# Kernel optimization log

Measured on AMD Instinct MI355X. Metric: run time of the kernel, lower is better.

The kernel has to match this reference:

```python
import jax, jax.numpy as jnp
import numpy as np

N_QUBITS = 14
LAYERS = 2
BATCH = 64
N_PARAMS = 5 * N_QUBITS * LAYERS  # 140
TWO_PI = 2.0 * np.pi
C64 = jnp.complex64


def _rx(t):  # t: [B] -> [B,2,2]
    c = jnp.cos(t * 0.5).astype(C64)
    s = (-1j * jnp.sin(t * 0.5)).astype(C64)
    return jnp.stack([jnp.stack([c, s], -1), jnp.stack([s, c], -1)], -2)


def _ry(t):
    c = jnp.cos(t * 0.5).astype(C64)
    s = jnp.sin(t * 0.5).astype(C64)
    return jnp.stack([jnp.stack([c, -s], -1), jnp.stack([s, c], -1)], -2)


def _rz(t):
    e = jnp.exp(-0.5j * t.astype(C64))
    z = jnp.zeros_like(e)
    return jnp.stack([jnp.stack([e, z], -1), jnp.stack([z, jnp.conj(e)], -1)], -2)


def _apply_1q(psi, U, axis):
    # psi: [B, 2, 2, ...]; U: [B,2,2]; apply U on given tensor axis (>=1).
    psi = jnp.moveaxis(psi, axis, -1)
    psi = jnp.einsum('b...j,bij->b...i', psi, U)
    return jnp.moveaxis(psi, -1, axis)


def _apply_crx(psi, theta, ctrl, tgt):
    # controlled-RX: apply RX(theta) on target only in the control=1 subspace.
    U = _rx(theta)
    psi0 = jax.lax.index_in_dim(psi, 0, axis=ctrl + 1, keepdims=False)
    psi1 = jax.lax.index_in_dim(psi, 1, axis=ctrl + 1, keepdims=False)
    t2 = tgt if tgt < ctrl else tgt - 1  # target axis after removing ctrl axis
    psi1 = _apply_1q(psi1, U, t2 + 1)
    return jnp.stack([psi0, psi1], axis=ctrl + 1)


def _circuit(angles):
    # angles: [B, N_PARAMS] -> features [B, 3*N_QUBITS] (X, Y, Z expvals)
    B = angles.shape[0]
    n = N_QUBITS
    psi = jnp.zeros((B, 2 ** n), C64).at[:, 0].set(1.0)
    psi = psi.reshape((B,) + (2,) * n)
    idx = 0
    for _ in range(LAYERS):
        for i in range(n):
            psi = _apply_1q(psi, _rx(angles[:, idx]), i + 1)
            psi = _apply_1q(psi, _ry(angles[:, idx + 1]), i + 1)
            psi = _apply_1q(psi, _rz(angles[:, idx + 2]), i + 1)
            idx += 3
        for i in range(n):  # forward CRX ring
            psi = _apply_crx(psi, angles[:, idx], i, (i + 1) % n)
            idx += 1
        for i in range(n - 1, -1, -1):  # backward CRX ring
            psi = _apply_crx(psi, angles[:, idx], i, (i - 1) % n)
            idx += 1
    conj = jnp.conj(psi)
    probs = jnp.real(psi * conj)
    axes_all = tuple(range(1, n + 1))
    xs, ys, zs = [], [], []
    for w in range(n):
        flip = jnp.flip(psi, axis=w + 1)  # X action: swap |0>,|1> on wire w
        xs.append(jnp.real(jnp.sum(conj * flip, axis=axes_all)))
        fshape = [1] * (n + 1)
        fshape[w + 1] = 2
        f = jnp.array([-1j, 1j], C64).reshape(fshape)  # Y phases
        ys.append(jnp.real(jnp.sum(conj * f * flip, axis=axes_all)))
        p = probs.sum(axis=tuple(a for a in axes_all if a != w + 1))  # [B,2]
        zs.append(p[:, 0] - p[:, 1])
    return jnp.stack(xs + ys + zs, axis=1).astype(jnp.float32)


def setup_inputs() -> dict:
    key = jax.random.key(0)
    k1, k2 = jax.random.split(key)
    params = jax.random.normal(k1, (BATCH, N_PARAMS), dtype=jnp.float32)
    base_params = jax.random.uniform(k2, (N_PARAMS,), dtype=jnp.float32) * TWO_PI
    return {"params": params, "base_params": base_params}


def reference(params, base_params):
    angles = jax.nn.sigmoid(params + base_params[None, :]) * TWO_PI
    return _circuit(angles)
```

## Files before the change

### kernel.cpp

```cpp
#include <hip/hip_runtime.h>

#define NP 140
#define NT 1024

typedef float2 f2;

__device__ __forceinline__ float sigmoid2pi(float x) {
    return 6.28318530717958647692f / (1.0f + __expf(-x));
}
__device__ __forceinline__ f2 cmulf(f2 a, f2 b) {
    return make_float2(a.x * b.x - a.y * b.y, a.x * b.y + a.y * b.x);
}
__device__ __forceinline__ f2 comb(f2 ca, f2 m, f2 cb, f2 o) {
    return make_float2(ca.x * m.x - ca.y * m.y + cb.x * o.x - cb.y * o.y,
                       ca.x * m.y + ca.y * m.x + cb.x * o.y + cb.y * o.x);
}
__device__ __forceinline__ f2 rxmix(float ch, float sh, f2 m, f2 o) {
    return make_float2(ch * m.x + sh * o.y, ch * m.y - sh * o.x);
}
__device__ __forceinline__ float wsum(float v) {
    v += __shfl_down(v, 32); v += __shfl_down(v, 16); v += __shfl_down(v, 8);
    v += __shfl_down(v, 4);  v += __shfl_down(v, 2);  v += __shfl_down(v, 1);
    return v;
}

constexpr unsigned rot14c(unsigned x, int d) {
    return ((x << d) | (x >> (14 - d))) & 16383u;
}
constexpr unsigned koffc(unsigned i, int d) {
    unsigned c = rot14c(i, d);
    return (c + (c >> 4) + (c >> 8)) * 8u;
}

#define P_B0(OP) OP(0,1) OP(2,3) OP(4,5) OP(6,7) OP(8,9) OP(10,11) OP(12,13) OP(14,15)
#define P_B1(OP) OP(0,2) OP(1,3) OP(4,6) OP(5,7) OP(8,10) OP(9,11) OP(12,14) OP(13,15)
#define P_B2(OP) OP(0,4) OP(1,5) OP(2,6) OP(3,7) OP(8,12) OP(9,13) OP(10,14) OP(11,15)
#define P_B3(OP) OP(0,8) OP(1,9) OP(2,10) OP(3,11) OP(4,12) OP(5,13) OP(6,14) OP(7,15)
#define P_32(OP) OP(8,12) OP(9,13) OP(10,14) OP(11,15)
#define P_21(OP) OP(4,6) OP(5,7) OP(12,14) OP(13,15)
#define P_10(OP) OP(2,3) OP(6,7) OP(10,11) OP(14,15)
#define P_23(OP) OP(4,12) OP(5,13) OP(6,14) OP(7,15)
#define P_12(OP) OP(2,6) OP(3,7) OP(10,14) OP(11,15)
#define P_01(OP) OP(1,3) OP(5,7) OP(9,11) OP(13,15)

#define OP_RX(a_, b_) { f2 ta_ = st##a_; \
    st##a_ = rxmix(ch_, sh_, ta_, st##b_); st##b_ = rxmix(ch_, sh_, st##b_, ta_); }
#define OP_G1(a_, b_) { f2 ta_ = st##a_, tb_ = st##b_; \
    st##a_ = comb(u00_, ta_, u01_, tb_); st##b_ = comb(u10_, ta_, u11_, tb_); }
#define OP_MX(a_, b_) { \
    sx += st##a_.x * st##b_.x + st##a_.y * st##b_.y; \
    sy += st##a_.x * st##b_.y - st##a_.y * st##b_.x; \
    sz += st##a_.x * st##a_.x + st##a_.y * st##a_.y - st##b_.x * st##b_.x - st##b_.y * st##b_.y; }

#define CRX_CL(CI_, PL) { f2 cs_ = csh2[CI_]; float ch_ = cs_.x, sh_ = cs_.y; PL(OP_RX) }
#define CRX_SEL0(CI_) { f2 cs_ = csh2[CI_]; float ch_ = cs_.x, sh_ = cs_.y; \
    if (tid & 1) { P_B3(OP_RX) } }
#define CRX_W512(CI_) { f2 cs_ = csh2[CI_]; float ch_ = cs_.x, sh_ = cs_.y; \
    if (tid & 512) { P_B0(OP_RX) } }
#define G1Q(q_, PL) { float4 ga_ = g1v[q_][0], gb_ = g1v[q_][1]; \
    f2 u00_ = make_float2(ga_.x, ga_.y), u01_ = make_float2(ga_.z, ga_.w); \
    f2 u10_ = make_float2(gb_.x, gb_.y), u11_ = make_float2(gb_.z, gb_.w); PL(OP_G1) }
#define MEAS(w_, PL) { float sx = 0.f, sy = 0.f, sz = 0.f; PL(OP_MX) \
    sx = wsum(2.f * sx); sy = wsum(2.f * sy); sz = wsum(sz); \
    if ((tid & 63) == 0) { red[w_][tid >> 6][0] = sx; red[w_][tid >> 6][1] = sy; red[w_][tid >> 6][2] = sz; } }

#define XPOSE(D_) { \
    __syncthreads(); \
    { char* wb_ = (char*)exb + (unsigned)(tid * 17 + (tid >> 4)) * 8u; \
      *(f2*)(wb_ +   0) = st0;  *(f2*)(wb_ +   8) = st1;  *(f2*)(wb_ +  16) = st2;  *(f2*)(wb_ +  24) = st3; \
      *(f2*)(wb_ +  32) = st4;  *(f2*)(wb_ +  40) = st5;  *(f2*)(wb_ +  48) = st6;  *(f2*)(wb_ +  56) = st7; \
      *(f2*)(wb_ +  64) = st8;  *(f2*)(wb_ +  72) = st9;  *(f2*)(wb_ +  80) = st10; *(f2*)(wb_ +  88) = st11; \
      *(f2*)(wb_ +  96) = st12; *(f2*)(wb_ + 104) = st13; *(f2*)(wb_ + 112) = st14; *(f2*)(wb_ + 120) = st15; } \
    __syncthreads(); \
    { unsigned aw_ = (unsigned)tid << 4; \
      unsigned rt_ = ((aw_ << (D_)) | (aw_ >> (14 - (D_)))) & 16383u; \
      const char* rb_ = (const char*)exb + (rt_ + (rt_ >> 4) + (rt_ >> 8)) * 8u; \
      st0  = *(const f2*)(rb_ + koffc(0,  D_)); st1  = *(const f2*)(rb_ + koffc(1,  D_)); \
      st2  = *(const f2*)(rb_ + koffc(2,  D_)); st3  = *(const f2*)(rb_ + koffc(3,  D_)); \
      st4  = *(const f2*)(rb_ + koffc(4,  D_)); st5  = *(const f2*)(rb_ + koffc(5,  D_)); \
      st6  = *(const f2*)(rb_ + koffc(6,  D_)); st7  = *(const f2*)(rb_ + koffc(7,  D_)); \
      st8  = *(const f2*)(rb_ + koffc(8,  D_)); st9  = *(const f2*)(rb_ + koffc(9,  D_)); \
      st10 = *(const f2*)(rb_ + koffc(10, D_)); st11 = *(const f2*)(rb_ + koffc(11, D_)); \
      st12 = *(const f2*)(rb_ + koffc(12, D_)); st13 = *(const f2*)(rb_ + koffc(13, D_)); \
      st14 = *(const f2*)(rb_ + koffc(14, D_)); st15 = *(const f2*)(rb_ + koffc(15, D_)); } }

__global__
__attribute__((amdgpu_flat_work_group_size(1024, 1024), amdgpu_waves_per_eu(4, 4)))
void qfe_kernel(const float* __restrict__ params,
                const float* __restrict__ base,
                float* __restrict__ out)
{
    __shared__ f2 exb[17472];
    __shared__ f2 v1c[14][2];
    __shared__ float4 g1v[14][2];
    __shared__ f2 csh2[56];
    __shared__ float red[14][16][3];

    const int b = blockIdx.x;
    const int tid = threadIdx.x;

    if (tid < 14) {
        int q = tid, a = 3 * q;
        float t1 = sigmoid2pi(params[b * NP + a] + base[a]);
        float t2 = sigmoid2pi(params[b * NP + a + 1] + base[a + 1]);
        float t3 = sigmoid2pi(params[b * NP + a + 2] + base[a + 2]);
        float s1, c1, s2, c2, s3, c3;
        __sincosf(0.5f * t1, &s1, &c1);
        __sincosf(0.5f * t2, &s2, &c2);
        __sincosf(0.5f * t3, &s3, &c3);
        f2 m00 = make_float2(c2 * c1, s2 * s1);
        f2 m10 = make_float2(s2 * c1, -c2 * s1);
        f2 em = make_float2(c3, -s3), ep = make_float2(c3, s3);
        v1c[q][0] = cmulf(em, m00);
        v1c[q][1] = cmulf(ep, m10);
    } else if (tid >= 64 && tid < 78) {
        int q = tid - 64, a = 70 + 3 * q;
        float t1 = sigmoid2pi(params[b * NP + a] + base[a]);
        float t2 = sigmoid2pi(params[b * NP + a + 1] + base[a + 1]);
        float t3 = sigmoid2pi(params[b * NP + a + 2] + base[a + 2]);
        float s1, c1, s2, c2, s3, c3;
        __sincosf(0.5f * t1, &s1, &c1);
        __sincosf(0.5f * t2, &s2, &c2);
        __sincosf(0.5f * t3, &s3, &c3);
        f2 m00 = make_float2(c2 * c1, s2 * s1);
        f2 m01 = make_float2(-s2 * c1, -c2 * s1);
        f2 m10 = make_float2(s2 * c1, -c2 * s1);
        f2 m11 = make_float2(c2 * c1, -s2 * s1);
        f2 em = make_float2(c3, -s3), ep = make_float2(c3, s3);
        f2 u00 = cmulf(em, m00), u01 = cmulf(em, m01);
        f2 u10 = cmulf(ep, m10), u11 = cmulf(ep, m11);
        g1v[q][0] = make_float4(u00.x, u00.y, u01.x, u01.y);
        g1v[q][1] = make_float4(u10.x, u10.y, u11.x, u11.y);
    } else if (tid >= 128 && tid < 184) {
        int s = tid - 128;
        int layer = s / 28, k = s % 28;
        int aidx = layer * 70 + (k < 14 ? 42 + k : 56 + (k - 14));
        float th = sigmoid2pi(params[b * NP + aidx] + base[aidx]);
        float sh, ch;
        __sincosf(0.5f * th, &sh, &ch);
        csh2[s] = make_float2(ch, sh);
    }
    __syncthreads();

    f2 F = v1c[0][tid & 1];
    F = cmulf(F, v1c[13][(tid >> 1) & 1]);
    F = cmulf(F, v1c[12][(tid >> 2) & 1]);
    F = cmulf(F, v1c[11][(tid >> 3) & 1]);
    F = cmulf(F, v1c[10][(tid >> 4) & 1]);
    F = cmulf(F, v1c[9][(tid >> 5) & 1]);
    F = cmulf(F, v1c[8][(tid >> 6) & 1]);
    F = cmulf(F, v1c[7][(tid >> 7) & 1]);
    F = cmulf(F, v1c[6][(tid >> 8) & 1]);
    F = cmulf(F, v1c[5][(tid >> 9) & 1]);

    f2 st0, st1, st2, st3, st4, st5, st6, st7, st8, st9, st10, st11, st12, st13, st14, st15;
    st0 = cmulf(F, v1c[1][0]);  st8 = cmulf(F, v1c[1][1]);
    st4 = cmulf(st0, v1c[2][1]); st12 = cmulf(st8, v1c[2][1]);
    st0 = cmulf(st0, v1c[2][0]); st8  = cmulf(st8, v1c[2][0]);
    st2  = cmulf(st0, v1c[3][1]); st6  = cmulf(st4,  v1c[3][1]);
    st10 = cmulf(st8, v1c[3][1]); st14 = cmulf(st12, v1c[3][1]);
    st0  = cmulf(st0, v1c[3][0]); st4  = cmulf(st4,  v1c[3][0]);
    st8  = cmulf(st8, v1c[3][0]); st12 = cmulf(st12, v1c[3][0]);
    st1  = cmulf(st0,  v1c[4][1]); st3  = cmulf(st2,  v1c[4][1]);
    st5  = cmulf(st4,  v1c[4][1]); st7  = cmulf(st6,  v1c[4][1]);
    st9  = cmulf(st8,  v1c[4][1]); st11 = cmulf(st10, v1c[4][1]);
    st13 = cmulf(st12, v1c[4][1]); st15 = cmulf(st14, v1c[4][1]);
    st0  = cmulf(st0,  v1c[4][0]); st2  = cmulf(st2,  v1c[4][0]);
    st4  = cmulf(st4,  v1c[4][0]); st6  = cmulf(st6,  v1c[4][0]);
    st8  = cmulf(st8,  v1c[4][0]); st10 = cmulf(st10, v1c[4][0]);
    st12 = cmulf(st12, v1c[4][0]); st14 = cmulf(st14, v1c[4][0]);

    CRX_SEL0(0) CRX_CL(1, P_32) CRX_CL(2, P_21) CRX_CL(3, P_10)
    XPOSE(10)
    CRX_SEL0(4) CRX_CL(5, P_32) CRX_CL(6, P_21) CRX_CL(7, P_10)
    XPOSE(10)
    CRX_SEL0(8) CRX_CL(9, P_32) CRX_CL(10, P_21) CRX_CL(11, P_10)
    XPOSE(11)
    CRX_CL(12, P_32) CRX_CL(13, P_21) CRX_CL(14, P_23)
    XPOSE(3)
    CRX_CL(15, P_01) CRX_CL(16, P_12) CRX_CL(17, P_23)
    XPOSE(4)
    CRX_W512(18) CRX_CL(19, P_01) CRX_CL(20, P_12) CRX_CL(21, P_23)
    XPOSE(4)
    CRX_W512(22) CRX_CL(23, P_01) CRX_CL(24, P_12) CRX_CL(25, P_23)
    XPOSE(4)
    CRX_W512(26) CRX_CL(27, P_01)

    G1Q(0, P_B0) G1Q(13, P_B1) G1Q(12, P_B2) G1Q(11, P_B3)
    XPOSE(10)
    G1Q(1, P_B3) G1Q(2, P_B2) G1Q(3, P_B1) G1Q(4, P_B0)
    CRX_SEL0(28) CRX_CL(29, P_32) CRX_CL(30, P_21) CRX_CL(31, P_10)
    XPOSE(10)
    G1Q(5, P_B3) G1Q(6, P_B2) G1Q(7, P_B1) G1Q(8, P_B0)
    CRX_SEL0(32) CRX_CL(33, P_32) CRX_CL(34, P_21) CRX_CL(35, P_10)
    XPOSE(10)
    G1Q(9, P_B3) G1Q(10, P_B2)
    CRX_SEL0(36) CRX_CL(37, P_32) CRX_CL(38, P_21) CRX_CL(39, P_10)
    XPOSE(11)
    CRX_CL(40, P_32) CRX_CL(41, P_21) CRX_CL(42, P_23)
    XPOSE(3)
    CRX_CL(43, P_01) CRX_CL(44, P_12) CRX_CL(45, P_23)
    XPOSE(4)
    CRX_W512(46) CRX_CL(47, P_01) CRX_CL(48, P_12) CRX_CL(49, P_23)
    XPOSE(4)
    CRX_W512(50) CRX_CL(51, P_01) CRX_CL(52, P_12) CRX_CL(53, P_23)
    XPOSE(4)
    CRX_W512(54) CRX_CL(55, P_01)

    MEAS(0, P_B0) MEAS(13, P_B1) MEAS(12, P_B2) MEAS(11, P_B3)
    XPOSE(10)
    MEAS(1, P_B3) MEAS(2, P_B2) MEAS(3, P_B1) MEAS(4, P_B0)
    XPOSE(10)
    MEAS(5, P_B3) MEAS(6, P_B2) MEAS(7, P_B1) MEAS(8, P_B0)
    XPOSE(10)
    MEAS(9, P_B3) MEAS(10, P_B2)

    __syncthreads();
    if (tid < 42) {
        int comp = tid / 14, w = tid % 14;
        float s = 0.f;
        #pragma unroll
        for (int k = 0; k < 16; ++k) s += red[w][k][comp];
        out[b * 42 + comp * 14 + w] = s;
    }
}

extern "C" void kernel_launch(void* const* d_in, const int* in_sizes, int n_in,
                              void* d_out, int out_size, void* d_ws, size_t ws_size,
                              hipStream_t stream) {
    const float* params = (const float*)d_in[0];
    const float* base   = (const float*)d_in[1];
    float* out = (float*)d_out;
    const int B = in_sizes[0] / NP;
    qfe_kernel<<<B, NT, 0, stream>>>(params, base, out);
}
```

Baseline: 70.84 us.

## Use DPP lane exchanges for low-lane qubits to cut LDS transposes

```diff
diff --git a/kernel.cpp b/kernel.cpp
--- a/kernel.cpp
+++ b/kernel.cpp
@@ -18,9 +18,33 @@
 __device__ __forceinline__ f2 rxmix(float ch, float sh, f2 m, f2 o) {
     return make_float2(ch * m.x + sh * o.y, ch * m.y - sh * o.x);
 }
+__device__ __forceinline__ float rfl(float x) {
+    return __int_as_float(__builtin_amdgcn_readfirstlane(__float_as_int(x)));
+}
+
+#define XOR1 0xB1
+#define XOR2 0x4E
+#define XOR8 0x128
+template<int CTRL>
+__device__ __forceinline__ float xdpp(float v) {
+    return __int_as_float(__builtin_amdgcn_update_dpp(0, __float_as_int(v), CTRL, 0xF, 0xF, true));
+}
+template<int CTRL>
+__device__ __forceinline__ f2 xchg(f2 v) { return make_float2(xdpp<CTRL>(v.x), xdpp<CTRL>(v.y)); }
+__device__ __forceinline__ f2 xchg4(f2 v) {
+    return make_float2(
+        __int_as_float(__builtin_amdgcn_ds_swizzle(__float_as_int(v.x), 0x101F)),
+        __int_as_float(__builtin_amdgcn_ds_swizzle(__float_as_int(v.y), 0x101F)));
+}
+
+template<int CTRL>
+__device__ __forceinline__ float dppadd(float v) {
+    int t = __builtin_amdgcn_update_dpp(0, __float_as_int(v), CTRL, 0xF, 0xF, true);
+    return v + __int_as_float(t);
+}
 __device__ __forceinline__ float wsum(float v) {
-    v += __shfl_down(v, 32); v += __shfl_down(v, 16); v += __shfl_down(v, 8);
-    v += __shfl_down(v, 4);  v += __shfl_down(v, 2);  v += __shfl_down(v, 1);
+    v = dppadd<0x118>(v); v = dppadd<0x114>(v); v = dppadd<0x112>(v);
+    v = dppadd<0x111>(v); v = dppadd<0x142>(v); v = dppadd<0x143>(v);
     return v;
 }
 
@@ -42,27 +66,57 @@
 #define P_23(OP) OP(4,12) OP(5,13) OP(6,14) OP(7,15)
 #define P_12(OP) OP(2,6) OP(3,7) OP(10,14) OP(11,15)
 #define P_01(OP) OP(1,3) OP(5,7) OP(9,11) OP(13,15)
+#define ALL16(OP) OP(0) OP(1) OP(2) OP(3) OP(4) OP(5) OP(6) OP(7) OP(8) OP(9) OP(10) OP(11) OP(12) OP(13) OP(14) OP(15)
+#define HI8(OP)  OP(8) OP(9) OP(10) OP(11) OP(12) OP(13) OP(14) OP(15)
 
 #define OP_RX(a_, b_) { f2 ta_ = st##a_; \
     st##a_ = rxmix(ch_, sh_, ta_, st##b_); st##b_ = rxmix(ch_, sh_, st##b_, ta_); }
+#define OP_RXD(i_) { f2 o_ = xchg<CT_>(st##i_); st##i_ = rxmix(chx_, shx_, st##i_, o_); }
 #define OP_G1(a_, b_) { f2 ta_ = st##a_, tb_ = st##b_; \
     st##a_ = comb(u00_, ta_, u01_, tb_); st##b_ = comb(u10_, ta_, u11_, tb_); }
+#define OP_G1D(i_) { f2 o_ = xchg<CT_>(st##i_); st##i_ = comb(ca_, st##i_, cb_, o_); }
+
+#define CRX_LL(CI_, PL) { f2 cs_ = csh2[CI_]; float ch_ = rfl(cs_.x), sh_ = rfl(cs_.y); PL(OP_RX) }
+#define CRX_SELC(CI_, SELM_, PL) { f2 cs_ = csh2[CI_]; \
+    float ch_ = (tid & SELM_) ? cs_.x : 1.0f, sh_ = (tid & SELM_) ? cs_.y : 0.0f; PL(OP_RX) }
+#define CRX_SELW(CI_, PL) { f2 cs_ = csh2[CI_]; float ch_ = rfl(cs_.x), sh_ = rfl(cs_.y); \
+    if (tid & 512) { PL(OP_RX) } }
+#define CRX_DPPSEL(CI_, SELM_, CTV_) { f2 cs_ = csh2[CI_]; \
+    float chx_ = (tid & SELM_) ? cs_.x : 1.0f, shx_ = (tid & SELM_) ? cs_.y : 0.0f; \
+    constexpr int CT_ = CTV_; ALL16(OP_RXD) }
+#define CRX_DPPH8(CI_, CTV_) { f2 cs_ = csh2[CI_]; \
+    float chx_ = rfl(cs_.x), shx_ = rfl(cs_.y); \
+    constexpr int CT_ = CTV_; HI8(OP_RXD) }
+#define G1Q(q_, PL) { float4 ga_ = g1v[q_][0], gb_ = g1v[q_][1]; \
+    f2 u00_ = make_float2(ga_.x, ga_.y), u01_ = make_float2(ga_.z, ga_.w); \
+    f2 u10_ = make_float2(gb_.x, gb_.y), u11_ = make_float2(gb_.z, gb_.w); PL(OP_G1) }
+#define G1QL(q_, CTV_, SELM_) { float4 ga_ = g1v[q_][0], gb_ = g1v[q_][1]; \
+    f2 u00_ = make_float2(ga_.x, ga_.y), u01_ = make_float2(ga_.z, ga_.w); \
+    f2 u10_ = make_float2(gb_.x, gb_.y), u11_ = make_float2(gb_.z, gb_.w); \
+    f2 ca_ = (tid & SELM_) ? u11_ : u00_, cb_ = (tid & SELM_) ? u10_ : u01_; \
+    constexpr int CT_ = CTV_; ALL16(OP_G1D) }
+
+#define RED_STORE(W_) { \
+    sx = wsum(sx); sy = wsum(sy); sz = wsum(sz); \
+    if ((tid & 63) == 63) { red[W_][tid >> 6][0] = sx; red[W_][tid >> 6][1] = sy; red[W_][tid >> 6][2] = sz; } }
 #define OP_MX(a_, b_) { \
     sx += st##a_.x * st##b_.x + st##a_.y * st##b_.y; \
     sy += st##a_.x * st##b_.y - st##a_.y * st##b_.x; \
     sz += st##a_.x * st##a_.x + st##a_.y * st##a_.y - st##b_.x * st##b_.x - st##b_.y * st##b_.y; }
-
-#define CRX_CL(CI_, PL) { f2 cs_ = csh2[CI_]; float ch_ = cs_.x, sh_ = cs_.y; PL(OP_RX) }
-#define CRX_SEL0(CI_) { f2 cs_ = csh2[CI_]; float ch_ = cs_.x, sh_ = cs_.y; \
-    if (tid & 1) { P_B3(OP_RX) } }
-#define CRX_W512(CI_) { f2 cs_ = csh2[CI_]; float ch_ = cs_.x, sh_ = cs_.y; \
-    if (tid & 512) { P_B0(OP_RX) } }
-#define G1Q(q_, PL) { float4 ga_ = g1v[q_][0], gb_ = g1v[q_][1]; \
-    f2 u00_ = make_float2(ga_.x, ga_.y), u01_ = make_float2(ga_.z, ga_.w); \
-    f2 u10_ = make_float2(gb_.x, gb_.y), u11_ = make_float2(gb_.z, gb_.w); PL(OP_G1) }
-#define MEAS(w_, PL) { float sx = 0.f, sy = 0.f, sz = 0.f; PL(OP_MX) \
-    sx = wsum(2.f * sx); sy = wsum(2.f * sy); sz = wsum(sz); \
-    if ((tid & 63) == 0) { red[w_][tid >> 6][0] = sx; red[w_][tid >> 6][1] = sy; red[w_][tid >> 6][2] = sz; } }
+#define OP_MD(i_) { f2 o_ = xchg<CT_>(st##i_); \
+    sx += st##i_.x * o_.x + st##i_.y * o_.y; \
+    sy += sg_ * (st##i_.x * o_.y - st##i_.y * o_.x); \
+    sz += sg_ * (st##i_.x * st##i_.x + st##i_.y * st##i_.y); }
+#define OP_MS(i_) { f2 o_ = xchg4(st##i_); \
+    sx += st##i_.x * o_.x + st##i_.y * o_.y; \
+    sy += sg_ * (st##i_.x * o_.y - st##i_.y * o_.x); \
+    sz += sg_ * (st##i_.x * st##i_.x + st##i_.y * st##i_.y); }
+#define MEAS_LOC(w_, PL) { float sx = 0.f, sy = 0.f, sz = 0.f; PL(OP_MX) \
+    sx *= 2.f; sy *= 2.f; RED_STORE(w_) }
+#define MEAS_D(w_, CTV_, SGM_) { constexpr int CT_ = CTV_; float sg_ = (tid & SGM_) ? -1.f : 1.f; \
+    float sx = 0.f, sy = 0.f, sz = 0.f; ALL16(OP_MD) RED_STORE(w_) }
+#define MEAS_SWZ(w_, SGM_) { float sg_ = (tid & SGM_) ? -1.f : 1.f; \
+    float sx = 0.f, sy = 0.f, sz = 0.f; ALL16(OP_MS) RED_STORE(w_) }
 
 #define XPOSE(D_) { \
     __syncthreads(); \
@@ -77,10 +131,13 @@
       const char* rb_ = (const char*)exb + (rt_ + (rt_ >> 4) + (rt_ >> 8)) * 8u; \
       st0  = *(const f2*)(rb_ + koffc(0,  D_)); st1  = *(const f2*)(rb_ + koffc(1,  D_)); \
       st2  = *(const f2*)(rb_ + koffc(2,  D_)); st3  = *(const f2*)(rb_ + koffc(3,  D_)); \
+      __builtin_amdgcn_sched_barrier(0); \
       st4  = *(const f2*)(rb_ + koffc(4,  D_)); st5  = *(const f2*)(rb_ + koffc(5,  D_)); \
       st6  = *(const f2*)(rb_ + koffc(6,  D_)); st7  = *(const f2*)(rb_ + koffc(7,  D_)); \
+      __builtin_amdgcn_sched_barrier(0); \
       st8  = *(const f2*)(rb_ + koffc(8,  D_)); st9  = *(const f2*)(rb_ + koffc(9,  D_)); \
       st10 = *(const f2*)(rb_ + koffc(10, D_)); st11 = *(const f2*)(rb_ + koffc(11, D_)); \
+      __builtin_amdgcn_sched_barrier(0); \
       st12 = *(const f2*)(rb_ + koffc(12, D_)); st13 = *(const f2*)(rb_ + koffc(13, D_)); \
       st14 = *(const f2*)(rb_ + koffc(14, D_)); st15 = *(const f2*)(rb_ + koffc(15, D_)); } }
 
@@ -142,78 +199,91 @@
     }
     __syncthreads();
 
-    f2 F = v1c[0][tid & 1];
-    F = cmulf(F, v1c[13][(tid >> 1) & 1]);
-    F = cmulf(F, v1c[12][(tid >> 2) & 1]);
-    F = cmulf(F, v1c[11][(tid >> 3) & 1]);
-    F = cmulf(F, v1c[10][(tid >> 4) & 1]);
-    F = cmulf(F, v1c[9][(tid >> 5) & 1]);
-    F = cmulf(F, v1c[8][(tid >> 6) & 1]);
-    F = cmulf(F, v1c[7][(tid >> 7) & 1]);
-    F = cmulf(F, v1c[6][(tid >> 8) & 1]);
-    F = cmulf(F, v1c[5][(tid >> 9) & 1]);
+    f2 F = v1c[12][tid & 1];
+    F = cmulf(F, v1c[11][(tid >> 1) & 1]);
+    F = cmulf(F, v1c[10][(tid >> 2) & 1]);
+    F = cmulf(F, v1c[9][(tid >> 3) & 1]);
+    F = cmulf(F, v1c[8][(tid >> 4) & 1]);
+    F = cmulf(F, v1c[7][(tid >> 5) & 1]);
+    F = cmulf(F, v1c[6][(tid >> 6) & 1]);
+    F = cmulf(F, v1c[5][(tid >> 7) & 1]);
+    F = cmulf(F, v1c[4][(tid >> 8) & 1]);
+    F = cmulf(F, v1c[3][(tid >> 9) & 1]);
 
     f2 st0, st1, st2, st3, st4, st5, st6, st7, st8, st9, st10, st11, st12, st13, st14, st15;
-    st0 = cmulf(F, v1c[1][0]);  st8 = cmulf(F, v1c[1][1]);
-    st4 = cmulf(st0, v1c[2][1]); st12 = cmulf(st8, v1c[2][1]);
-    st0 = cmulf(st0, v1c[2][0]); st8  = cmulf(st8, v1c[2][0]);
-    st2  = cmulf(st0, v1c[3][1]); st6  = cmulf(st4,  v1c[3][1]);
-    st10 = cmulf(st8, v1c[3][1]); st14 = cmulf(st12, v1c[3][1]);
-    st0  = cmulf(st0, v1c[3][0]); st4  = cmulf(st4,  v1c[3][0]);
-    st8  = cmulf(st8, v1c[3][0]); st12 = cmulf(st12, v1c[3][0]);
-    st1  = cmulf(st0,  v1c[4][1]); st3  = cmulf(st2,  v1c[4][1]);
-    st5  = cmulf(st4,  v1c[4][1]); st7  = cmulf(st6,  v1c[4][1]);
-    st9  = cmulf(st8,  v1c[4][1]); st11 = cmulf(st10, v1c[4][1]);
-    st13 = cmulf(st12, v1c[4][1]); st15 = cmulf(st14, v1c[4][1]);
-    st0  = cmulf(st0,  v1c[4][0]); st2  = cmulf(st2,  v1c[4][0]);
-    st4  = cmulf(st4,  v1c[4][0]); st6  = cmulf(st6,  v1c[4][0]);
-    st8  = cmulf(st8,  v1c[4][0]); st10 = cmulf(st10, v1c[4][0]);
-    st12 = cmulf(st12, v1c[4][0]); st14 = cmulf(st14, v1c[4][0]);
-
-    CRX_SEL0(0) CRX_CL(1, P_32) CRX_CL(2, P_21) CRX_CL(3, P_10)
-    XPOSE(10)
-    CRX_SEL0(4) CRX_CL(5, P_32) CRX_CL(6, P_21) CRX_CL(7, P_10)
-    XPOSE(10)
-    CRX_SEL0(8) CRX_CL(9, P_32) CRX_CL(10, P_21) CRX_CL(11, P_10)
-    XPOSE(11)
-    CRX_CL(12, P_32) CRX_CL(13, P_21) CRX_CL(14, P_23)
-    XPOSE(3)
-    CRX_CL(15, P_01) CRX_CL(16, P_12) CRX_CL(17, P_23)
-    XPOSE(4)
-    CRX_W512(18) CRX_CL(19, P_01) CRX_CL(20, P_12) CRX_CL(21, P_23)
-    XPOSE(4)
-    CRX_W512(22) CRX_CL(23, P_01) CRX_CL(24, P_12) CRX_CL(25, P_23)
-    XPOSE(4)
-    CRX_W512(26) CRX_CL(27, P_01)
-
-    G1Q(0, P_B0) G1Q(13, P_B1) G1Q(12, P_B2) G1Q(11, P_B3)
-    XPOSE(10)
-    G1Q(1, P_B3) G1Q(2, P_B2) G1Q(3, P_B1) G1Q(4, P_B0)
-    CRX_SEL0(28) CRX_CL(29, P_32) CRX_CL(30, P_21) CRX_CL(31, P_10)
-    XPOSE(10)
+    st0 = cmulf(F, v1c[13][0]); st8 = cmulf(F, v1c[13][1]);
+    st4 = cmulf(st0, v1c[0][1]); st12 = cmulf(st8, v1c[0][1]);
+    st0 = cmulf(st0, v1c[0][0]); st8  = cmulf(st8, v1c[0][0]);
+    st2  = cmulf(st0, v1c[1][1]); st6  = cmulf(st4,  v1c[1][1]);
+    st10 = cmulf(st8, v1c[1][1]); st14 = cmulf(st12, v1c[1][1]);
+    st0  = cmulf(st0, v1c[1][0]); st4  = cmulf(st4,  v1c[1][0]);
+    st8  = cmulf(st8, v1c[1][0]); st12 = cmulf(st12, v1c[1][0]);
+    st1  = cmulf(st0,  v1c[2][1]); st3  = cmulf(st2,  v1c[2][1]);
+    st5  = cmulf(st4,  v1c[2][1]); st7  = cmulf(st6,  v1c[2][1]);
+    st9  = cmulf(st8,  v1c[2][1]); st11 = cmulf(st10, v1c[2][1]);
+    st13 = cmulf(st12, v1c[2][1]); st15 = cmulf(st14, v1c[2][1]);
+    st0  = cmulf(st0,  v1c[2][0]); st2  = cmulf(st2,  v1c[2][0]);
+    st4  = cmulf(st4,  v1c[2][0]); st6  = cmulf(st6,  v1c[2][0]);
+    st8  = cmulf(st8,  v1c[2][0]); st10 = cmulf(st10, v1c[2][0]);
+    st12 = cmulf(st12, v1c[2][0]); st14 = cmulf(st14, v1c[2][0]);
+
+    CRX_LL(0, P_21) CRX_LL(1, P_10)
+    XPOSE(8)
+    CRX_DPPSEL(2, 4, XOR2)
+    CRX_DPPSEL(3, 2, XOR1)
+    CRX_SELC(4, 1, P_B3)
+    CRX_LL(5, P_32)
+    CRX_LL(6, P_21)
+    CRX_LL(7, P_10)
+    XPOSE(8)
+    CRX_DPPSEL(8, 4, XOR2)
+    CRX_DPPSEL(9, 2, XOR1)
+    CRX_SELC(10, 1, P_B3)
+    CRX_LL(11, P_32)
+    CRX_LL(12, P_21)
+    CRX_LL(13, P_10)
+    CRX_LL(14, P_12)
+    CRX_LL(15, P_23)
+    CRX_DPPH8(16, XOR1)
+    CRX_DPPSEL(17, 1, XOR2)
+    XPOSE(6)
+    CRX_SELW(18, P_B0)
+    CRX_LL(19, P_01)
+    CRX_LL(20, P_12)
+    CRX_LL(21, P_23)
+    CRX_DPPH8(22, XOR1)
+    CRX_DPPSEL(23, 1, XOR2)
+    XPOSE(6)
+    CRX_SELW(24, P_B0)
+    CRX_LL(25, P_01)
+    CRX_LL(26, P_12)
+    CRX_LL(27, P_23)
+
+    G1Q(13, P_B3) G1Q(0, P_B2) G1Q(1, P_B1) G1Q(2, P_B0)
+    G1QL(12, XOR1, 1) G1QL(11, XOR2, 2)
+    CRX_LL(28, P_21) CRX_LL(29, P_10)
+    XPOSE(8)
     G1Q(5, P_B3) G1Q(6, P_B2) G1Q(7, P_B1) G1Q(8, P_B0)
-    CRX_SEL0(32) CRX_CL(33, P_32) CRX_CL(34, P_21) CRX_CL(35, P_10)
-    XPOSE(10)
-    G1Q(9, P_B3) G1Q(10, P_B2)
-    CRX_SEL0(36) CRX_CL(37, P_32) CRX_CL(38, P_21) CRX_CL(39, P_10)
-    XPOSE(11)
-    CRX_CL(40, P_32) CRX_CL(41, P_21) CRX_CL(42, P_23)
-    XPOSE(3)
-    CRX_CL(43, P_01) CRX_CL(44, P_12) CRX_CL(45, P_23)
-    XPOSE(4)
-    CRX_W512(46) CRX_CL(47, P_01) CRX_CL(48, P_12) CRX_CL(49, P_23)
-    XPOSE(4)
-    CRX_W512(50) CRX_CL(51, P_01) CRX_CL(52, P_12) CRX_CL(53, P_23)
-    XPOSE(4)
-    CRX_W512(54) CRX_CL(55, P_01)
-
-    MEAS(0, P_B0) MEAS(13, P_B1) MEAS(12, P_B2) MEAS(11, P_B3)
-    XPOSE(10)
-    MEAS(1, P_B3) MEAS(2, P_B2) MEAS(3, P_B1) MEAS(4, P_B0)
-    XPOSE(10)
-    MEAS(5, P_B3) MEAS(6, P_B2) MEAS(7, P_B1) MEAS(8, P_B0)
-    XPOSE(10)
-    MEAS(9, P_B3) MEAS(10, P_B2)
+    G1QL(4, XOR1, 1) G1QL(3, XOR2, 2)
+    CRX_DPPSEL(30, 4, XOR2) CRX_DPPSEL(31, 2, XOR1) CRX_SELC(32, 1, P_B3)
+    CRX_LL(33, P_32) CRX_LL(34, P_21) CRX_LL(35, P_10)
+    XPOSE(8)
+    G1QL(10, XOR1, 1) G1QL(9, XOR2, 2)
+    CRX_DPPSEL(36, 4, XOR2) CRX_DPPSEL(37, 2, XOR1) CRX_SELC(38, 1, P_B3)
+    CRX_LL(39, P_32) CRX_LL(40, P_21) CRX_LL(41, P_10)
+    CRX_LL(42, P_12) CRX_LL(43, P_23) CRX_DPPH8(44, XOR1) CRX_DPPSEL(45, 1, XOR2)
+    XPOSE(6)
+    CRX_SELW(46, P_B0) CRX_LL(47, P_01) CRX_LL(48, P_12) CRX_LL(49, P_23)
+    CRX_DPPH8(50, XOR1) CRX_DPPSEL(51, 1, XOR2)
+    XPOSE(6)
+    CRX_SELW(52, P_B0) CRX_LL(53, P_01) CRX_LL(54, P_12) CRX_LL(55, P_23)
+
+    MEAS_LOC(2, P_B0) MEAS_LOC(1, P_B1) MEAS_LOC(0, P_B2) MEAS_LOC(13, P_B3)
+    MEAS_D(12, XOR1, 1) MEAS_D(11, XOR2, 2) MEAS_D(9, XOR8, 8)
+    MEAS_SWZ(10, 4)
+    XPOSE(8)
+    MEAS_LOC(8, P_B0) MEAS_LOC(7, P_B1) MEAS_LOC(6, P_B2) MEAS_LOC(5, P_B3)
+    MEAS_D(4, XOR1, 1) MEAS_D(3, XOR2, 2)
 
     __syncthreads();
     if (tid < 42) {
```

After: 74.23 us. 4.8% more time.
